# Kernel optimization log

Measured on AMD Instinct MI355X. Metric: run time of the kernel, lower is better.

The kernel has to match this reference:

```python
import jax, jax.numpy as jnp
import numpy as np

G = 32          # grid_size
H = 12          # num_heads
D = 768         # embed_dim
HD = D // H     # head_dim = 64
FF = 3072       # ff_dim
B, T = 2, 2048
SPAN = 2 * G - 1        # 63
SPAN_C = 4 * G + 1      # 129
EPS = 1e-5


def setup_inputs() -> dict:
    key = jax.random.key(0)
    ks = jax.random.split(key, 16)
    s = 0.02
    is_sep = jax.random.uniform(ks[6], (T,)) < 0.05
    demo_id = jax.random.randint(ks[5], (T,), 0, 8)
    demo_id = jnp.where(is_sep, -1, demo_id)
    return {
        'x': jax.random.normal(ks[0], (B, T, D), jnp.float32),
        'row': jax.random.randint(ks[1], (T,), 0, G),
        'col': jax.random.randint(ks[2], (T,), 0, G),
        'demo_row': jax.random.randint(ks[3], (T,), 0, G),
        'demo_col': jax.random.randint(ks[4], (T,), 0, 2 * G),
        'demo_id': demo_id,
        'is_sep': is_sep,
        'ln1_w': jnp.ones((D,), jnp.float32),
        'ln1_b': jnp.zeros((D,), jnp.float32),
        'ln2_w': jnp.ones((D,), jnp.float32),
        'ln2_b': jnp.zeros((D,), jnp.float32),
        'qkv_w': jax.random.normal(ks[7], (D, 3 * D), jnp.float32) * s,
        'qkv_b': jnp.zeros((3 * D,), jnp.float32),
        'proj_w': jax.random.normal(ks[8], (D, D), jnp.float32) * s,
        'proj_b': jnp.zeros((D,), jnp.float32),
        'ff1_w': jax.random.normal(ks[9], (D, FF), jnp.float32) * s,
        'ff1_b': jnp.zeros((FF,), jnp.float32),
        'ff2_w': jax.random.normal(ks[10], (FF, D), jnp.float32) * s,
        'ff2_b': jnp.zeros((D,), jnp.float32),
        'rel_emb': jax.random.normal(ks[11], (SPAN * SPAN, H), jnp.float32) * s,
        'demo_emb': jax.random.normal(ks[12], (SPAN_C * SPAN, H), jnp.float32) * s,
    }


def _ln(x, w, b):
    m = jnp.mean(x, -1, keepdims=True)
    v = jnp.mean((x - m) ** 2, -1, keepdims=True)
    return (x - m) / jnp.sqrt(v + EPS) * w + b


def _rel_bias(rel_emb, row, col, is_sep):
    g1 = G - 1
    dr = jnp.clip(row[:, None] - row[None, :], -g1, g1) + g1
    dc = jnp.clip(col[:, None] - col[None, :], -g1, g1) + g1
    bias = rel_emb[dr * SPAN + dc]              # (T, T, H)
    valid = ~is_sep
    vp = (valid[:, None] & valid[None, :]).astype(jnp.float32)
    return jnp.transpose(bias, (2, 0, 1)) * vp[None]  # (H, T, T)


def _demo_bias(demo_emb, drow, dcol, did, is_sep):
    g1 = G - 1
    dr = jnp.clip(drow[:, None] - drow[None, :], -g1, g1) + g1
    dc = jnp.clip(dcol[:, None] - dcol[None, :], -2 * G, 2 * G) + 2 * G
    bias = demo_emb[dr * SPAN_C + dc]           # (T, T, H)
    valid = ~is_sep
    same = (did[:, None] == did[None, :]) & (did[:, None] >= 0) & (did[None, :] >= 0)
    vp = (valid[:, None] & valid[None, :] & same).astype(jnp.float32)
    return jnp.transpose(bias, (2, 0, 1)) * vp[None]


def reference(x, row, col, demo_row, demo_col, demo_id, is_sep,
              ln1_w, ln1_b, ln2_w, ln2_b, qkv_w, qkv_b, proj_w, proj_b,
              ff1_w, ff1_b, ff2_w, ff2_b, rel_emb, demo_emb):
    b, t, d = x.shape
    h1 = _ln(x, ln1_w, ln1_b)
    qkv = h1 @ qkv_w + qkv_b                        # (B, T, 3D)
    q, k, v = jnp.split(qkv, 3, axis=-1)
    q = q.reshape(b, t, H, HD).transpose(0, 2, 1, 3)  # (B, H, T, HD)
    k = k.reshape(b, t, H, HD).transpose(0, 2, 1, 3)
    v = v.reshape(b, t, H, HD).transpose(0, 2, 1, 3)
    scale = float(HD) ** -0.5
    logits = jnp.einsum('bhqd,bhkd->bhqk', q, k) * scale
    bias = _rel_bias(rel_emb, row, col, is_sep) + _demo_bias(demo_emb, demo_row, demo_col, demo_id, is_sep)
    attn = jax.nn.softmax(logits + bias[None], axis=-1)
    out = jnp.einsum('bhqk,bhkd->bhqd', attn, v)
    out = out.transpose(0, 2, 1, 3).reshape(b, t, D)
    out = out @ proj_w + proj_b
    x = x + out
    h2 = _ln(x, ln2_w, ln2_b)
    ff = jax.nn.gelu(h2 @ ff1_w + ff1_b, approximate=False) @ ff2_w + ff2_b
    return x + ff
```

## Files before the change

kernel.cpp:

```cpp
#include <hip/hip_runtime.h>
#include <hip/hip_bf16.h>
#include <math.h>

#define G_ 32
#define H_ 12
#define D_ 768
#define HD_ 64
#define FF_ 3072
#define B_ 2
#define T_ 2048
#define SPAN_ 63
#define SPANC_ 129
#define EPSF 1e-5f

typedef short bf16x8 __attribute__((ext_vector_type(8)));
typedef short short4v __attribute__((ext_vector_type(4)));
typedef float f32x4 __attribute__((ext_vector_type(4)));

__device__ __forceinline__ short f2bf(float f) {
    unsigned u = __builtin_bit_cast(unsigned, f);
    u = u + 0x7FFFu + ((u >> 16) & 1u);
    return (short)(u >> 16);
}

__device__ __forceinline__ void gl_lds16(const void* g, void* l) {
    __builtin_amdgcn_global_load_lds(
        (const __attribute__((address_space(1))) unsigned int*)g,
        (__attribute__((address_space(3))) unsigned int*)l, 16, 0, 0);
}

__global__ __launch_bounds__(256) void ln_bf16_kernel(const float* __restrict__ x,
                                                      const float* __restrict__ w,
                                                      const float* __restrict__ b,
                                                      short* __restrict__ out) {
    int wv = threadIdx.x >> 6;
    int lane = threadIdx.x & 63;
    int rowi = blockIdx.x * 4 + wv;
    const float* xr = x + (size_t)rowi * D_;
    float vals[12];
    float s = 0.f;
#pragma unroll
    for (int i = 0; i < 12; ++i) { vals[i] = xr[lane + i * 64]; s += vals[i]; }
#pragma unroll
    for (int off = 32; off > 0; off >>= 1) s += __shfl_xor(s, off, 64);
    float mean = s * (1.0f / D_);
    float vs = 0.f;
#pragma unroll
    for (int i = 0; i < 12; ++i) { float d = vals[i] - mean; vs += d * d; }
#pragma unroll
    for (int off = 32; off > 0; off >>= 1) vs += __shfl_xor(vs, off, 64);
    float rstd = rsqrtf(vs * (1.0f / D_) + EPSF);
    short* outr = out + (size_t)rowi * D_;
#pragma unroll
    for (int i = 0; i < 12; ++i) {
        int c = lane + i * 64;
        outr[c] = f2bf((vals[i] - mean) * rstd * w[c] + b[c]);
    }
}

__global__ __launch_bounds__(256) void tcast_kernel(const float* __restrict__ W,
                                                    short* __restrict__ Wt,
                                                    int K, int N) {
    __shared__ float t[32][33];
    int n0 = blockIdx.x * 32, k0 = blockIdx.y * 32;
    int tid = threadIdx.x;
    int r = tid >> 3, c4 = (tid & 7) * 4;
    float4 v = *(const float4*)(W + (size_t)(k0 + r) * N + n0 + c4);
    t[r][c4 + 0] = v.x; t[r][c4 + 1] = v.y; t[r][c4 + 2] = v.z; t[r][c4 + 3] = v.w;
    __syncthreads();
    short4v o;
    o[0] = f2bf(t[c4 + 0][r]); o[1] = f2bf(t[c4 + 1][r]);
    o[2] = f2bf(t[c4 + 2][r]); o[3] = f2bf(t[c4 + 3][r]);
    *(short4v*)(Wt + (size_t)(n0 + r) * K + k0 + c4) = o;
}

__global__ __launch_bounds__(256) void bias_build(
    const int* __restrict__ rowp, const int* __restrict__ colp,
    const int* __restrict__ drowp, const int* __restrict__ dcolp,
    const int* __restrict__ didp,
    const float* __restrict__ rel_emb, const float* __restrict__ demo_emb,
    ushort* __restrict__ biasT) {
    __shared__ ushort patch[12][16][72];
    int k0 = blockIdx.x * 64, q0 = blockIdx.y * 16;
    int tid = threadIdx.x;
    int qi = tid >> 4, kq = (tid & 15) * 4;
    int q = q0 + qi;
    int idq = didp[q];
    int rq = rowp[q], cq = colp[q], drq = drowp[q], dcq = dcolp[q];
#pragma unroll
    for (int j = 0; j < 4; ++j) {
        int k = k0 + kq + j;
        int idk = didp[k];
        float4 v0 = {0.f, 0.f, 0.f, 0.f}, v1 = v0, v2 = v0;
        if (idq >= 0 && idk >= 0) {
            int dr = min(max(rq - rowp[k], -(G_ - 1)), G_ - 1) + (G_ - 1);
            int dc = min(max(cq - colp[k], -(G_ - 1)), G_ - 1) + (G_ - 1);
            const float* rp = rel_emb + (size_t)(dr * SPAN_ + dc) * 12;
            v0 = *(const float4*)rp;
            v1 = *(const float4*)(rp + 4);
            v2 = *(const float4*)(rp + 8);
            if (idq == idk) {
                int ddr = min(max(drq - drowp[k], -(G_ - 1)), G_ - 1) + (G_ - 1);
                int ddc = min(max(dcq - dcolp[k], -2 * G_), 2 * G_) + 2 * G_;
                const float* dp = demo_emb + (size_t)(ddr * SPANC_ + ddc) * 12;
                float4 w0 = *(const float4*)dp;
                float4 w1 = *(const float4*)(dp + 4);
                float4 w2 = *(const float4*)(dp + 8);
                v0.x += w0.x; v0.y += w0.y; v0.z += w0.z; v0.w += w0.w;
                v1.x += w1.x; v1.y += w1.y; v1.z += w1.z; v1.w += w1.w;
                v2.x += w2.x; v2.y += w2.y; v2.z += w2.z; v2.w += w2.w;
            }
        }
        float bv[12] = {v0.x, v0.y, v0.z, v0.w, v1.x, v1.y, v1.z, v1.w,
                        v2.x, v2.y, v2.z, v2.w};
        int kl = kq + j;
#pragma unroll
        for (int h = 0; h < 12; ++h) patch[h][qi][kl] = (ushort)f2bf(bv[h]);
    }
    __syncthreads();
    for (int c = tid; c < 1536; c += 256) {
        int rowid = c >> 3, off = (c & 7) * 8;
        int h = rowid >> 4, q2 = rowid & 15;
        *(bf16x8*)(biasT + (size_t)h * T_ * T_ + (size_t)(q0 + q2) * T_ + k0 + off) =
            *(const bf16x8*)&patch[h][q2][off];
    }
}

enum { EPI_NONE = 0, EPI_RES = 1, EPI_GELU = 2 };

template <int EPI, int BF16OUT>
__global__ __launch_bounds__(256, 2) void gemm_bf16(const short* __restrict__ A,
                                                    const short* __restrict__ Bt,
                                                    const float* __restrict__ bias,
                                                    const float* __restrict__ res,
                                                    void* __restrict__ Cv,
                                                    int M, int N, int K) {
    __shared__ short As[128 * 64];
    __shared__ short Bs[128 * 64];
    int tid = threadIdx.x;
    int l = tid & 63;
    int w = tid >> 6;
    int wm = w >> 1, wn = w & 1;
    int row0 = blockIdx.y * 128, col0 = blockIdx.x * 128;
    int g = l >> 4, c16 = l & 15;
    f32x4 zero = {0.f, 0.f, 0.f, 0.f};
    f32x4 acc[4][4];
#pragma unroll
    for (int m = 0; m < 4; ++m)
#pragma unroll
        for (int n = 0; n < 4; ++n) acc[m][n] = zero;

    int srow = w * 32 + (l >> 3);
    int sseg0 = (l & 7);

    for (int k0 = 0; k0 < K; k0 += 64) {
#pragma unroll
        for (int inst = 0; inst < 4; ++inst) {
            int arow = srow + inst * 8;
            int seg = sseg0 ^ (arow & 7);
            gl_lds16(A + (size_t)(row0 + arow) * K + k0 + seg * 8,
                     &As[(w * 32 + inst * 8) * 64]);
            gl_lds16(Bt + (size_t)(col0 + arow) * K + k0 + seg * 8,
                     &Bs[(w * 32 + inst * 8) * 64]);
        }
        __syncthreads();
#pragma unroll
        for (int dk = 0; dk < 2; ++dk) {
            bf16x8 af[4], bfr[4];
#pragma unroll
            for (int m = 0; m < 4; ++m) {
                int r = wm * 64 + m * 16 + c16;
                af[m] = *(const bf16x8*)&As[r * 64 + (((dk * 4 + g) ^ (r & 7)) << 3)];
            }
#pragma unroll
            for (int n = 0; n < 4; ++n) {
                int r = wn * 64 + n * 16 + c16;
                bfr[n] = *(const bf16x8*)&Bs[r * 64 + (((dk * 4 + g) ^ (r & 7)) << 3)];
            }
#pragma unroll
            for (int m = 0; m < 4; ++m)
#pragma unroll
                for (int n = 0; n < 4; ++n)
                    acc[m][n] = __builtin_amdgcn_mfma_f32_16x16x32_bf16(af[m], bfr[n], acc[m][n], 0, 0, 0);
        }
        __syncthreads();
    }

#pragma unroll
    for (int m = 0; m < 4; ++m)
#pragma unroll
        for (int n = 0; n < 4; ++n) {
            int rrow = row0 + wm * 64 + m * 16 + g * 4;
            int ccol = col0 + wn * 64 + n * 16 + c16;
            float bv = bias[ccol];
#pragma unroll
            for (int i = 0; i < 4; ++i) {
                float v = acc[m][n][i] + bv;
                if (EPI == EPI_GELU) v = 0.5f * v * (1.f + erff(v * 0.70710678118f));
                if (EPI == EPI_RES) v += res[(size_t)(rrow + i) * N + ccol];
                if (BF16OUT)
                    ((short*)Cv)[(size_t)(rrow + i) * N + ccol] = f2bf(v);
                else
                    ((float*)Cv)[(size_t)(rrow + i) * N + ccol] = v;
            }
        }
}

__global__ __launch_bounds__(256, 2) void attn_mfma(
    const short* __restrict__ qkv,
    const ushort* __restrict__ biasT,
    short* __restrict__ attn_o) {
    __shared__ short Ks[2][64 * 64];
    __shared__ short Vt[2][64 * 72];
    __shared__ short Pb[4][16 * 72];

    int tid = threadIdx.x, w = tid >> 6, l = tid & 63;
    int g = l >> 4, c16 = l & 15;
    int qt = blockIdx.x & 31, bh = blockIdx.x >> 5;
    int h = bh % H_, b = bh / H_;
    int q0 = qt * 64;
    const int QS = 3 * D_;
    const short* kvbase = qkv + (size_t)b * T_ * QS;

    bf16x8 qf[2];
    {
        int qrow = q0 + w * 16 + c16;
        const short* qp = kvbase + (size_t)qrow * QS + h * HD_;
        qf[0] = *(const bf16x8*)(qp + g * 8);
        qf[1] = *(const bf16x8*)(qp + 32 + g * 8);
    }
    const ushort* bptr[4];
#pragma unroll
    for (int i = 0; i < 4; ++i)
        bptr[i] = biasT + (size_t)h * T_ * T_ + (size_t)(q0 + w * 16 + g * 4 + i) * T_;

    int krow = tid >> 3, kseg = tid & 7;
    int kx = (kseg ^ (krow & 7)) << 3;
    const short* kgp = kvbase + D_ + h * HD_ + kseg * 8;
    int vk0 = (tid & 31) * 2, vd0 = (tid >> 5) * 8;
    int vbase = ((((vk0 >> 3) ^ (vd0 >> 3)) & 7) << 3) + (vk0 & 7);
    const short* vgp = kvbase + 2 * D_ + h * HD_ + vd0;

    f32x4 zero = {0.f, 0.f, 0.f, 0.f};
    f32x4 oacc[4];
#pragma unroll
    for (int nf = 0; nf < 4; ++nf) oacc[nf] = zero;
    float lsum[4] = {0.f, 0.f, 0.f, 0.f};

    bf16x8 kr0, kr1, vr0, vr1;
    kr0 = *(const bf16x8*)(kgp + (size_t)krow * QS);
    kr1 = *(const bf16x8*)(kgp + (size_t)(krow + 32) * QS);
    vr0 = *(const bf16x8*)(vgp + (size_t)vk0 * QS);
    vr1 = *(const bf16x8*)(vgp + (size_t)(vk0 + 1) * QS);
    *(bf16x8*)&Ks[0][krow * 64 + kx] = kr0;
    *(bf16x8*)&Ks[0][(krow + 32) * 64 + kx] = kr1;
#pragma unroll
    for (int j = 0; j < 8; ++j) {
        unsigned pr = (unsigned)(ushort)vr0[j] | ((unsigned)(ushort)vr1[j] << 16);
        *(unsigned*)&Vt[0][(vd0 + j) * 72 + vbase] = pr;
    }
    {
        const short* kg1 = kgp + (size_t)64 * QS;
        const short* vg1 = vgp + (size_t)64 * QS;
        kr0 = *(const bf16x8*)(kg1 + (size_t)krow * QS);
        kr1 = *(const bf16x8*)(kg1 + (size_t)(krow + 32) * QS);
        vr0 = *(const bf16x8*)(vg1 + (size_t)vk0 * QS);
        vr1 = *(const bf16x8*)(vg1 + (size_t)(vk0 + 1) * QS);
    }

    for (int t = 0; t < 32; ++t) {
        __syncthreads();
        const short* KsC = Ks[t & 1];
        const short* VtC = Vt[t & 1];
        short* KsN = Ks[(t + 1) & 1];
        short* VtN = Vt[(t + 1) & 1];
        *(bf16x8*)&KsN[krow * 64 + kx] = kr0;
        *(bf16x8*)&KsN[(krow + 32) * 64 + kx] = kr1;
#pragma unroll
        for (int j = 0; j < 8; ++j) {
            unsigned pr = (unsigned)(ushort)vr0[j] | ((unsigned)(ushort)vr1[j] << 16);
            *(unsigned*)&VtN[(vd0 + j) * 72 + vbase] = pr;
        }
        {
            int kb2 = ((t + 2) & 31) * 64;
            const short* kg2 = kgp + (size_t)kb2 * QS;
            const short* vg2 = vgp + (size_t)kb2 * QS;
            kr0 = *(const bf16x8*)(kg2 + (size_t)krow * QS);
            kr1 = *(const bf16x8*)(kg2 + (size_t)(krow + 32) * QS);
            vr0 = *(const bf16x8*)(vg2 + (size_t)vk0 * QS);
            vr1 = *(const bf16x8*)(vg2 + (size_t)(vk0 + 1) * QS);
        }
        int kb = t * 64;
        float bv[16];
#pragma unroll
        for (int nf = 0; nf < 4; ++nf)
#pragma unroll
            for (int i = 0; i < 4; ++i)
                bv[nf * 4 + i] =
                    __builtin_bit_cast(float, (unsigned)bptr[i][kb + nf * 16 + c16] << 16);
        f32x4 sac[4];
#pragma unroll
        for (int nf = 0; nf < 4; ++nf) sac[nf] = zero;
#pragma unroll
        for (int dk = 0; dk < 2; ++dk) {
#pragma unroll
            for (int nf = 0; nf < 4; ++nf) {
                int r = nf * 16 + c16;
                bf16x8 kf = *(const bf16x8*)&KsC[r * 64 + (((dk * 4 + g) ^ (r & 7)) << 3)];
                sac[nf] = __builtin_amdgcn_mfma_f32_16x16x32_bf16(qf[dk], kf, sac[nf], 0, 0, 0);
            }
        }
#pragma unroll
        for (int nf = 0; nf < 4; ++nf)
#pragma unroll
            for (int i = 0; i < 4; ++i) {
                float e = __expf(fmaf(sac[nf][i], 0.125f, bv[nf * 4 + i]));
                sac[nf][i] = e;
                lsum[i] += e;
            }
        short* pbw = &Pb[w][0];
#pragma unroll
        for (int nf = 0; nf < 4; ++nf) {
            int chunkbase = nf * 2 + (c16 >> 3);
            int kpos = c16 & 7;
#pragma unroll
            for (int i = 0; i < 4; ++i)
                pbw[(g * 4 + i) * 72 + (((chunkbase ^ g) & 7) << 3) + kpos] = f2bf(sac[nf][i]);
        }
#pragma unroll
        for (int dk = 0; dk < 2; ++dk) {
            bf16x8 pa = *(const bf16x8*)&pbw[c16 * 72 + (((dk * 4 + g) ^ (c16 >> 2)) & 7) * 8];
#pragma unroll
            for (int nf = 0; nf < 4; ++nf) {
                int d = nf * 16 + c16;
                bf16x8 vb = *(const bf16x8*)&VtC[d * 72 + (((dk * 4 + g) ^ (d >> 3)) & 7) * 8];
                oacc[nf] = __builtin_amdgcn_mfma_f32_16x16x32_bf16(pa, vb, oacc[nf], 0, 0, 0);
            }
        }
    }

#pragma unroll
    for (int i = 0; i < 4; ++i) {
#pragma unroll
        for (int off = 1; off < 16; off <<= 1) lsum[i] += __shfl_xor(lsum[i], off, 64);
    }

#pragma unroll
    for (int nf = 0; nf < 4; ++nf)
#pragma unroll
        for (int i = 0; i < 4; ++i) {
            float o = oacc[nf][i] / lsum[i];
            int qq = q0 + w * 16 + g * 4 + i;
            attn_o[(size_t)(b * T_ + qq) * D_ + h * HD_ + nf * 16 + c16] = f2bf(o);
        }
}

extern "C" void kernel_launch(void* const* d_in, const int* in_sizes, int n_in,
                              void* d_out, int out_size, void* d_ws, size_t ws_size,
                              hipStream_t stream) {
    const float* x = (const float*)d_in[0];
    const int* rowp = (const int*)d_in[1];
    const int* colp = (const int*)d_in[2];
    const int* drowp = (const int*)d_in[3];
    const int* dcolp = (const int*)d_in[4];
    const int* didp = (const int*)d_in[5];
    const float* ln1_w = (const float*)d_in[7];
    const float* ln1_b = (const float*)d_in[8];
    const float* ln2_w = (const float*)d_in[9];
    const float* ln2_b = (const float*)d_in[10];
    const float* qkv_w = (const float*)d_in[11];
    const float* qkv_b = (const float*)d_in[12];
    const float* proj_w = (const float*)d_in[13];
    const float* proj_b = (const float*)d_in[14];
    const float* ff1_w = (const float*)d_in[15];
    const float* ff1_b = (const float*)d_in[16];
    const float* ff2_w = (const float*)d_in[17];
    const float* ff2_b = (const float*)d_in[18];
    const float* rel_emb = (const float*)d_in[19];
    const float* demo_emb = (const float*)d_in[20];
    float* out = (float*)d_out;

    const int M = B_ * T_;
    char* p = (char*)d_ws;
    short* h1 = (short*)p;     p += (size_t)M * D_ * 2;
    short* qkvb = (short*)p;   p += (size_t)M * 3 * D_ * 2;
    short* attn_o = (short*)p; p += (size_t)M * D_ * 2;
    short* qkvt = (short*)p;   p += (size_t)(3 * D_) * D_ * 2;
    short* projt = (short*)p;  p += (size_t)D_ * D_ * 2;
    short* ff1t = (short*)p;   p += (size_t)FF_ * D_ * 2;
    short* ff2t = (short*)p;   p += (size_t)D_ * FF_ * 2;
    float* x2 = (float*)p;
    short* h2 = (short*)(p + (size_t)M * D_ * 4);
    short* ffact = (short*)(p + (size_t)M * D_ * 4 + (size_t)M * D_ * 2);
    ushort* biasT = (ushort*)p;

    bias_build<<<dim3(T_ / 64, T_ / 16), 256, 0, stream>>>(
        rowp, colp, drowp, dcolp, didp, rel_emb, demo_emb, biasT);
    tcast_kernel<<<dim3(3 * D_ / 32, D_ / 32), 256, 0, stream>>>(qkv_w, qkvt, D_, 3 * D_);
    tcast_kernel<<<dim3(D_ / 32, D_ / 32), 256, 0, stream>>>(proj_w, projt, D_, D_);
    tcast_kernel<<<dim3(FF_ / 32, D_ / 32), 256, 0, stream>>>(ff1_w, ff1t, D_, FF_);
    tcast_kernel<<<dim3(D_ / 32, FF_ / 32), 256, 0, stream>>>(ff2_w, ff2t, FF_, D_);

    ln_bf16_kernel<<<dim3(M / 4), 256, 0, stream>>>(x, ln1_w, ln1_b, h1);

    gemm_bf16<EPI_NONE, 1><<<dim3(3 * D_ / 128, M / 128), 256, 0, stream>>>(
        h1, qkvt, qkv_b, nullptr, qkvb, M, 3 * D_, D_);

    attn_mfma<<<dim3(B_ * H_ * (T_ / 64)), 256, 0, stream>>>(qkvb, biasT, attn_o);

    gemm_bf16<EPI_RES, 0><<<dim3(D_ / 128, M / 128), 256, 0, stream>>>(
        attn_o, projt, proj_b, x, x2, M, D_, D_);

    ln_bf16_kernel<<<dim3(M / 4), 256, 0, stream>>>(x2, ln2_w, ln2_b, h2);

    gemm_bf16<EPI_GELU, 1><<<dim3(FF_ / 128, M / 128), 256, 0, stream>>>(
        h2, ff1t, ff1_b, nullptr, ffact, M, FF_, D_);

    gemm_bf16<EPI_RES, 0><<<dim3(D_ / 128, M / 128), 256, 0, stream>>>(
        ffact, ff2t, ff2_b, x2, out, M, D_, FF_);
}
```

Before: 262.9 us.

## Store attention bias in fp8 e5m2, shrink M tile for narrow GEMMs, remap attention blocks

The precomputed H×T×T attention bias is stored as 8-bit e5m2 instead of bf16, which halves the bytes bias_build writes and attn_mfma reads. The GEMM kernel gains a BM template parameter, and the two N=768 output GEMMs use 64-row tiles so more blocks are launched. The attention grid index is also permuted so consecutive blocks are spread across heads and query tiles. The fp8 bias keeps only two mantissa bits, which adds rounding error to the logits and could exceed tolerance.

```diff
diff --git a/kernel.cpp b/kernel.cpp
--- a/kernel.cpp
+++ b/kernel.cpp
@@ -1,5 +1,6 @@
 #include <hip/hip_runtime.h>
 #include <hip/hip_bf16.h>
+#include <hip/hip_fp16.h>
 #include <math.h>
 
 #define G_ 32
@@ -21,6 +22,15 @@
     unsigned u = __builtin_bit_cast(unsigned, f);
     u = u + 0x7FFFu + ((u >> 16) & 1u);
     return (short)(u >> 16);
+}
+
+__device__ __forceinline__ unsigned char f2e5m2(float f) {
+    unsigned short u = __half_as_ushort(__float2half(f));
+    u = (unsigned short)(u + 0x7F + ((u >> 8) & 1));
+    return (unsigned char)(u >> 8);
+}
+__device__ __forceinline__ float e5m2f(unsigned u) {
+    return __half2float(__ushort_as_half((unsigned short)(u << 8)));
 }
 
 __device__ __forceinline__ void gl_lds16(const void* g, void* l) {
@@ -79,14 +89,15 @@
     const int* __restrict__ drowp, const int* __restrict__ dcolp,
     const int* __restrict__ didp,
     const float* __restrict__ rel_emb, const float* __restrict__ demo_emb,
-    ushort* __restrict__ biasT) {
-    __shared__ ushort patch[12][16][72];
+    unsigned char* __restrict__ biasT) {
+    __shared__ unsigned char patch[12][16][80];
     int k0 = blockIdx.x * 64, q0 = blockIdx.y * 16;
     int tid = threadIdx.x;
     int qi = tid >> 4, kq = (tid & 15) * 4;
     int q = q0 + qi;
     int idq = didp[q];
     int rq = rowp[q], cq = colp[q], drq = drowp[q], dcq = dcolp[q];
+    float bvs[4][12];
 #pragma unroll
     for (int j = 0; j < 4; ++j) {
         int k = k0 + kq + j;
@@ -111,65 +122,78 @@
                 v2.x += w2.x; v2.y += w2.y; v2.z += w2.z; v2.w += w2.w;
             }
         }
-        float bv[12] = {v0.x, v0.y, v0.z, v0.w, v1.x, v1.y, v1.z, v1.w,
-                        v2.x, v2.y, v2.z, v2.w};
-        int kl = kq + j;
-#pragma unroll
-        for (int h = 0; h < 12; ++h) patch[h][qi][kl] = (ushort)f2bf(bv[h]);
+        bvs[j][0] = v0.x; bvs[j][1] = v0.y; bvs[j][2] = v0.z; bvs[j][3] = v0.w;
+        bvs[j][4] = v1.x; bvs[j][5] = v1.y; bvs[j][6] = v1.z; bvs[j][7] = v1.w;
+        bvs[j][8] = v2.x; bvs[j][9] = v2.y; bvs[j][10] = v2.z; bvs[j][11] = v2.w;
+    }
+#pragma unroll
+    for (int h = 0; h < 12; ++h) {
+        uchar4 pk;
+        pk.x = f2e5m2(bvs[0][h]); pk.y = f2e5m2(bvs[1][h]);
+        pk.z = f2e5m2(bvs[2][h]); pk.w = f2e5m2(bvs[3][h]);
+        *(uchar4*)&patch[h][qi][kq] = pk;
     }
     __syncthreads();
-    for (int c = tid; c < 1536; c += 256) {
-        int rowid = c >> 3, off = (c & 7) * 8;
+    for (int c = tid; c < 768; c += 256) {
+        int rowid = c >> 2, off = (c & 3) * 16;
         int h = rowid >> 4, q2 = rowid & 15;
-        *(bf16x8*)(biasT + (size_t)h * T_ * T_ + (size_t)(q0 + q2) * T_ + k0 + off) =
-            *(const bf16x8*)&patch[h][q2][off];
+        *(uint4*)(biasT + (size_t)h * T_ * T_ + (size_t)(q0 + q2) * T_ + k0 + off) =
+            *(const uint4*)&patch[h][q2][off];
     }
 }
 
 enum { EPI_NONE = 0, EPI_RES = 1, EPI_GELU = 2 };
 
-template <int EPI, int BF16OUT>
+template <int EPI, int BF16OUT, int BM>
 __global__ __launch_bounds__(256, 2) void gemm_bf16(const short* __restrict__ A,
                                                     const short* __restrict__ Bt,
                                                     const float* __restrict__ bias,
                                                     const float* __restrict__ res,
                                                     void* __restrict__ Cv,
                                                     int M, int N, int K) {
-    __shared__ short As[128 * 64];
+    __shared__ short As[BM * 64];
     __shared__ short Bs[128 * 64];
+    constexpr int WM = BM / 2;
+    constexpr int MF = WM / 16;
     int tid = threadIdx.x;
     int l = tid & 63;
     int w = tid >> 6;
     int wm = w >> 1, wn = w & 1;
-    int row0 = blockIdx.y * 128, col0 = blockIdx.x * 128;
+    int row0 = blockIdx.y * BM, col0 = blockIdx.x * 128;
     int g = l >> 4, c16 = l & 15;
     f32x4 zero = {0.f, 0.f, 0.f, 0.f};
-    f32x4 acc[4][4];
-#pragma unroll
-    for (int m = 0; m < 4; ++m)
+    f32x4 acc[MF][4];
+#pragma unroll
+    for (int m = 0; m < MF; ++m)
 #pragma unroll
         for (int n = 0; n < 4; ++n) acc[m][n] = zero;
 
-    int srow = w * 32 + (l >> 3);
+    int srowA = w * (BM / 4) + (l >> 3);
+    int srowB = w * 32 + (l >> 3);
     int sseg0 = (l & 7);
 
     for (int k0 = 0; k0 < K; k0 += 64) {
 #pragma unroll
-        for (int inst = 0; inst < 4; ++inst) {
-            int arow = srow + inst * 8;
+        for (int inst = 0; inst < BM / 32; ++inst) {
+            int arow = srowA + inst * 8;
             int seg = sseg0 ^ (arow & 7);
             gl_lds16(A + (size_t)(row0 + arow) * K + k0 + seg * 8,
-                     &As[(w * 32 + inst * 8) * 64]);
-            gl_lds16(Bt + (size_t)(col0 + arow) * K + k0 + seg * 8,
+                     &As[(w * (BM / 4) + inst * 8) * 64]);
+        }
+#pragma unroll
+        for (int inst = 0; inst < 4; ++inst) {
+            int brow = srowB + inst * 8;
+            int seg = sseg0 ^ (brow & 7);
+            gl_lds16(Bt + (size_t)(col0 + brow) * K + k0 + seg * 8,
                      &Bs[(w * 32 + inst * 8) * 64]);
         }
         __syncthreads();
 #pragma unroll
         for (int dk = 0; dk < 2; ++dk) {
-            bf16x8 af[4], bfr[4];
-#pragma unroll
-            for (int m = 0; m < 4; ++m) {
-                int r = wm * 64 + m * 16 + c16;
+            bf16x8 af[MF], bfr[4];
+#pragma unroll
+            for (int m = 0; m < MF; ++m) {
+                int r = wm * WM + m * 16 + c16;
                 af[m] = *(const bf16x8*)&As[r * 64 + (((dk * 4 + g) ^ (r & 7)) << 3)];
             }
 #pragma unroll
@@ -178,7 +202,7 @@
                 bfr[n] = *(const bf16x8*)&Bs[r * 64 + (((dk * 4 + g) ^ (r & 7)) << 3)];
             }
 #pragma unroll
-            for (int m = 0; m < 4; ++m)
+            for (int m = 0; m < MF; ++m)
 #pragma unroll
                 for (int n = 0; n < 4; ++n)
                     acc[m][n] = __builtin_amdgcn_mfma_f32_16x16x32_bf16(af[m], bfr[n], acc[m][n], 0, 0, 0);
@@ -187,10 +211,10 @@
     }
 
 #pragma unroll
-    for (int m = 0; m < 4; ++m)
+    for (int m = 0; m < MF; ++m)
 #pragma unroll
         for (int n = 0; n < 4; ++n) {
-            int rrow = row0 + wm * 64 + m * 16 + g * 4;
+            int rrow = row0 + wm * WM + m * 16 + g * 4;
             int ccol = col0 + wn * 64 + n * 16 + c16;
             float bv = bias[ccol];
 #pragma unroll
@@ -208,7 +232,7 @@
 
 __global__ __launch_bounds__(256, 2) void attn_mfma(
     const short* __restrict__ qkv,
-    const ushort* __restrict__ biasT,
+    const unsigned char* __restrict__ biasT,
     short* __restrict__ attn_o) {
     __shared__ short Ks[2][64 * 64];
     __shared__ short Vt[2][64 * 72];
@@ -216,7 +240,9 @@
 
     int tid = threadIdx.x, w = tid >> 6, l = tid & 63;
     int g = l >> 4, c16 = l & 15;
-    int qt = blockIdx.x & 31, bh = blockIdx.x >> 5;
+    int bid = blockIdx.x;
+    int nb = (bid & 7) * 96 + (bid >> 3);
+    int qt = nb & 31, bh = nb >> 5;
     int h = bh % H_, b = bh / H_;
     int q0 = qt * 64;
     const int QS = 3 * D_;
@@ -229,7 +255,7 @@
         qf[0] = *(const bf16x8*)(qp + g * 8);
         qf[1] = *(const bf16x8*)(qp + 32 + g * 8);
     }
-    const ushort* bptr[4];
+    const unsigned char* bptr[4];
 #pragma unroll
     for (int i = 0; i < 4; ++i)
         bptr[i] = biasT + (size_t)h * T_ * T_ + (size_t)(q0 + w * 16 + g * 4 + i) * T_;
@@ -296,8 +322,7 @@
         for (int nf = 0; nf < 4; ++nf)
 #pragma unroll
             for (int i = 0; i < 4; ++i)
-                bv[nf * 4 + i] =
-                    __builtin_bit_cast(float, (unsigned)bptr[i][kb + nf * 16 + c16] << 16);
+                bv[nf * 4 + i] = e5m2f(bptr[i][kb + nf * 16 + c16]);
         f32x4 sac[4];
 #pragma unroll
         for (int nf = 0; nf < 4; ++nf) sac[nf] = zero;
@@ -392,7 +417,7 @@
     float* x2 = (float*)p;
     short* h2 = (short*)(p + (size_t)M * D_ * 4);
     short* ffact = (short*)(p + (size_t)M * D_ * 4 + (size_t)M * D_ * 2);
-    ushort* biasT = (ushort*)p;
+    unsigned char* biasT = (unsigned char*)p;
 
     bias_build<<<dim3(T_ / 64, T_ / 16), 256, 0, stream>>>(
         rowp, colp, drowp, dcolp, didp, rel_emb, demo_emb, biasT);
@@ -403,19 +428,19 @@
 
     ln_bf16_kernel<<<dim3(M / 4), 256, 0, stream>>>(x, ln1_w, ln1_b, h1);
 
-    gemm_bf16<EPI_NONE, 1><<<dim3(3 * D_ / 128, M / 128), 256, 0, stream>>>(
+    gemm_bf16<EPI_NONE, 1, 128><<<dim3(3 * D_ / 128, M / 128), 256, 0, stream>>>(
         h1, qkvt, qkv_b, nullptr, qkvb, M, 3 * D_, D_);
 
     attn_mfma<<<dim3(B_ * H_ * (T_ / 64)), 256, 0, stream>>>(qkvb, biasT, attn_o);
 
-    gemm_bf16<EPI_RES, 0><<<dim3(D_ / 128, M / 128), 256, 0, stream>>>(
+    gemm_bf16<EPI_RES, 0, 64><<<dim3(D_ / 128, M / 64), 256, 0, stream>>>(
         attn_o, projt, proj_b, x, x2, M, D_, D_);
 
     ln_bf16_kernel<<<dim3(M / 4), 256, 0, stream>>>(x2, ln2_w, ln2_b, h2);
 
-    gemm_bf16<EPI_GELU, 1><<<dim3(FF_ / 128, M / 128), 256, 0, stream>>>(
+    gemm_bf16<EPI_GELU, 1, 128><<<dim3(FF_ / 128, M / 128), 256, 0, stream>>>(
         h2, ff1t, ff1_b, nullptr, ffact, M, FF_, D_);
 
-    gemm_bf16<EPI_RES, 0><<<dim3(D_ / 128, M / 128), 256, 0, stream>>>(
+    gemm_bf16<EPI_RES, 0, 64><<<dim3(D_ / 128, M / 64), 256, 0, stream>>>(
         ffact, ff2t, ff2_b, x2, out, M, D_, FF_);
 }
```

After: 242.9 us. 1.08x faster.
